# Optimization experiments

Measured on AMD Instinct MI355X. Metric: run time of the kernel, lower is better.

## Reference

```python
import jax, jax.numpy as jnp
import numpy as np

N = 10000   # num_nodes
E = 320000  # num_edges
D = 256     # feature / hidden dim
H = 256


def adj_lap(edge_index, n):
    """Dense normalized adjacency (gcn_norm, no self loops) and sym Laplacian."""
    row, col = edge_index[0], edge_index[1]
    # dense 0/1 adjacency (duplicate edges overwrite with same value, as in the loop)
    A = jnp.zeros((n, n), dtype=jnp.float32).at[row, col].set(1.0)
    # gcn_norm: deg = scatter(w, col) -> column sums
    deg_c = A.sum(axis=0)
    dinv_c = jnp.where(deg_c > 0, jax.lax.rsqrt(jnp.maximum(deg_c, 1e-12)), 0.0)
    anorm = dinv_c[:, None] * A * dinv_c[None, :]
    # get_laplacian 'sym': deg = scatter(w, row) -> row sums; L = I - D^-1/2 A D^-1/2
    deg_r = A.sum(axis=1)
    dinv_r = jnp.where(deg_r > 0, jax.lax.rsqrt(jnp.maximum(deg_r, 1e-12)), 0.0)
    lap = jnp.eye(n, dtype=jnp.float32) - dinv_r[:, None] * A * dinv_r[None, :]
    return lap, anorm


def gcn2(x, M, W1, b1, W2, b2):
    # pretrain_model: two-layer spectral GCN using propagation matrix M
    h = jax.nn.relu(M @ (x @ W1) + b1)
    return M @ (h @ W2) + b2


def setup_inputs() -> dict:
    key = jax.random.key(0)
    k1, k2, k3, k4 = jax.random.split(key, 4)
    x = jax.random.normal(k1, (N, D), dtype=jnp.float32)
    edge_index = jax.random.randint(k2, (2, E), 0, N, dtype=jnp.int64)
    W1 = jax.random.normal(k3, (D, H), dtype=jnp.float32) * 0.05
    b1 = jnp.zeros((H,), dtype=jnp.float32)
    W2 = jax.random.normal(k4, (H, H), dtype=jnp.float32) * 0.05
    b2 = jnp.zeros((H,), dtype=jnp.float32)
    return {"x": x, "edge_index": edge_index, "W1": W1, "b1": b1, "W2": W2, "b2": b2}


def reference(x, edge_index, W1, b1, W2, b2):
    # identity augmentor: x1 = x2 = x, edge_index1 = edge_index2 = edge_index,
    # so adj_lap is identical for both branches (computed once).
    lsym, anorm = adj_lap(edge_index, x.shape[0])
    z1 = gcn2(x, lsym, W1, b1, W2, b2)   # 'high' pass
    z2 = gcn2(x, anorm, W1, b1, W2, b2)  # 'low' pass
    z = z2
    return (z, z1, z2)
```

## Files before the change

### kernel.cpp

```cpp
#include <hip/hip_runtime.h>

#define NN 10000
#define EE 320000
#define HH 256
#define BKT 192

typedef __attribute__((ext_vector_type(8))) short bf16x8;
typedef __attribute__((ext_vector_type(4))) float f32x4;
typedef __attribute__((ext_vector_type(2))) float f32x2;

__device__ float bf2f(unsigned int v) {
    return __uint_as_float(v << 16);
}
__device__ unsigned short f2bf(float f) {
    unsigned int i = __float_as_uint(f);
    return (unsigned short)((i + 0x7fffu + ((i >> 16) & 1u)) >> 16);
}
__device__ unsigned int fp8e(float f) {
    float a = fabsf(f);
    a = fminf(a, 448.0f);
    unsigned int bits = __float_as_uint(a * __uint_as_float(0x03800000u));
    bits = bits + 0x7ffffu + ((bits >> 20) & 1u);
    unsigned int r = bits >> 20;
    if (r > 0x7eu) r = 0x7eu;
    return r | ((__float_as_uint(f) >> 24) & 0x80u);
}
__device__ float fp8d(unsigned int b) {
    float mag = __uint_as_float((b & 0x7fu) << 20) * __uint_as_float(0x7B800000u);
    return __uint_as_float(((b & 0x80u) << 24) | __float_as_uint(mag));
}
__device__ __forceinline__ void fp8dec4(unsigned int g, float* o) {
#if __has_builtin(__builtin_amdgcn_cvt_pk_f32_fp8)
    f32x2 lo = __builtin_amdgcn_cvt_pk_f32_fp8((int)g, false);
    f32x2 hi = __builtin_amdgcn_cvt_pk_f32_fp8((int)g, true);
    o[0] = lo.x; o[1] = lo.y; o[2] = hi.x; o[3] = hi.y;
#else
    #pragma unroll
    for (int j = 0; j < 4; j++) o[j] = fp8d((g >> (8 * j)) & 0xffu);
#endif
}
__device__ unsigned int pk2(unsigned short a, unsigned short b) {
    return (unsigned int)a | ((unsigned int)b << 16);
}
__device__ int eload(const void* ei, int is64, int idx) {
    if (is64) return (int)(((const long long*)ei)[idx]);
    return ((const int*)ei)[idx];
}
__device__ __forceinline__ float dinv_of(int d) {
    return d > 0 ? rsqrtf((float)d) : 0.0f;
}

__global__ void k_A(const void* x, const void* ei, const void* W1, const void* W2,
                    int* flags, int* rawcnt, unsigned short* W1sw,
                    unsigned short* W2sw) {
    int b = blockIdx.x, t = threadIdx.x;
    if (b >= 65) {
        int idx = (b - 65) * 256 + t;
        ((uint4*)rawcnt)[idx] = make_uint4(0, 0, 0, 0);
        return;
    }
    if (b == 0) {
        __shared__ int s0, s1;
        if (t == 0) { s0 = 0; s1 = 0; }
        __syncthreads();
        if (t < 64) {
            const unsigned int* eu = (const unsigned int*)ei;
            const unsigned int* xu = (const unsigned int*)x;
            for (int k = t; k < 256; k += 64)
                if (eu[2 * k + 1] != 0) atomicOr(&s0, 1);
            unsigned int lo = xu[t] & 0xffffu;
            unsigned int ex = (lo >> 7) & 0xffu;
            if (lo == 0u || (ex >= 90u && ex <= 150u)) atomicAdd(&s1, 1);
        }
        __syncthreads();
        if (t == 0) {
            flags[0] = s0 ? 0 : 1;
            flags[1] = (s1 >= 56) ? 0 : 1;
        }
        return;
    }
    __shared__ int plaus;
    if (t == 0) plaus = 0;
    __syncthreads();
    if (t < 64) {
        unsigned int lo = ((const unsigned int*)x)[t] & 0xffffu;
        unsigned int ex = (lo >> 7) & 0xffu;
        if (lo == 0u || (ex >= 90u && ex <= 150u)) atomicAdd(&plaus, 1);
    }
    __syncthreads();
    int f32io = (plaus >= 56) ? 0 : 1;
    int vb = b - 1;
    const void* W = (vb < 32) ? W1 : W2;
    unsigned short* O = (vb < 32) ? W1sw : W2sw;
    int g = ((vb < 32) ? vb : vb - 32) * 256 + t;
    int gl = g & 63;
    int n = (g >> 6) & 15;
    int ks = g >> 10;
    int coln = n * 16 + (gl & 15);
    int krow = ks * 32 + ((gl >> 4) & 3) * 8;
    unsigned short v[8];
    if (f32io) {
        const float* Wf = (const float*)W;
        #pragma unroll
        for (int j = 0; j < 8; j++) v[j] = f2bf(Wf[(size_t)(krow + j) * HH + coln]);
    } else {
        const unsigned short* Wh = (const unsigned short*)W;
        #pragma unroll
        for (int j = 0; j < 8; j++) v[j] = Wh[(size_t)(krow + j) * HH + coln];
    }
    uint4 p;
    p.x = pk2(v[0], v[1]); p.y = pk2(v[2], v[3]);
    p.z = pk2(v[4], v[5]); p.w = pk2(v[6], v[7]);
    *(uint4*)(O + (size_t)g * 8) = p;
}

__global__ void k_B(const void* x, const void* ei, const unsigned short* W1sw,
                    const int* flags, int* rawcnt, unsigned short* bucket,
                    unsigned char* Yf8, void* Oout) {
    int b = blockIdx.x;
    int tid = threadIdx.x;
    if (b >= 625) {
        int e = (b - 625) * 256 + tid;
        if (e >= EE) return;
        int is64 = flags[0];
        int r = eload(ei, is64, e);
        int c = eload(ei, is64, EE + e);
        if (r < 0 || r >= NN || c < 0 || c >= NN) return;
        int slot = atomicAdd(&rawcnt[r], 1);
        if (slot < BKT) bucket[(size_t)r * BKT + slot] = (unsigned short)c;
        return;
    }
    __shared__ unsigned short As[16][264];
    int r0 = b * 16;
    int af32 = flags[1];
    {
        int row = tid >> 4, seg = tid & 15;
        if (af32) {
            const float* ap = (const float*)x + (size_t)(r0 + row) * HH + seg * 16;
            unsigned short v[16];
            #pragma unroll
            for (int j = 0; j < 16; j += 4) {
                float4 q = *(const float4*)(ap + j);
                v[j] = f2bf(q.x); v[j + 1] = f2bf(q.y);
                v[j + 2] = f2bf(q.z); v[j + 3] = f2bf(q.w);
            }
            uint4 p0, p1;
            p0.x = pk2(v[0], v[1]);   p0.y = pk2(v[2], v[3]);
            p0.z = pk2(v[4], v[5]);   p0.w = pk2(v[6], v[7]);
            p1.x = pk2(v[8], v[9]);   p1.y = pk2(v[10], v[11]);
            p1.z = pk2(v[12], v[13]); p1.w = pk2(v[14], v[15]);
            *(uint4*)&As[row][seg * 16] = p0;
            *(uint4*)&As[row][seg * 16 + 8] = p1;
        } else {
            const unsigned short* ap = (const unsigned short*)x + (size_t)(r0 + row) * HH + seg * 16;
            *(uint4*)&As[row][seg * 16] = *(const uint4*)ap;
            *(uint4*)&As[row][seg * 16 + 8] = *(const uint4*)(ap + 8);
        }
    }
    __syncthreads();
    int wv = tid >> 6;
    int lane = tid & 63;
    int quad = lane >> 4;
    int l16 = lane & 15;
    f32x4 acc[4] = {{0,0,0,0},{0,0,0,0},{0,0,0,0},{0,0,0,0}};
    for (int ks = 0; ks < 8; ks++) {
        bf16x8 af = *(const bf16x8*)&As[l16][ks * 32 + quad * 8];
        #pragma unroll
        for (int t = 0; t < 4; t++) {
            int n = wv * 4 + t;
            bf16x8 bf = *(const bf16x8*)(W1sw + ((size_t)(ks * 16 + n) * 64 + lane) * 8);
            acc[t] = __builtin_amdgcn_mfma_f32_16x16x32_bf16(af, bf, acc[t], 0, 0, 0);
        }
    }
    size_t chunkW = (size_t)NN * HH;
    #pragma unroll
    for (int t = 0; t < 4; t++) {
        int cn = (wv * 4 + t) * 16 + l16;
        #pragma unroll
        for (int r = 0; r < 4; r++) {
            int row = r0 + quad * 4 + r;
            float vv = acc[t][r];
            size_t idx = (size_t)row * HH + cn;
            Yf8[idx] = (unsigned char)fp8e(vv);
            if (af32) ((float*)Oout)[2 * chunkW + idx] = vv;
            else      ((unsigned short*)Oout)[2 * chunkW + idx] = f2bf(vv);
        }
    }
}

__global__ void k_DD(const int* rawcnt, int* cnt2, unsigned short* bucket) {
    __shared__ unsigned int bm[4][316];
    __shared__ int cnt[4];
    int wave = threadIdx.x >> 6;
    int lane = threadIdx.x & 63;
    int i = blockIdx.x * 4 + wave;
    int d = rawcnt[i];
    if (d > BKT) d = BKT;
    for (int t = lane; t < 313; t += 64) bm[wave][t] = 0u;
    if (lane == 0) cnt[wave] = 0;
    unsigned short* bp = bucket + (size_t)i * BKT;
    int cvals[3];
    int nt = 0;
    for (int t = lane; t < d; t += 64) cvals[nt++] = (int)bp[t];
    for (int k = 0; k < nt; k++) {
        int c = cvals[k];
        unsigned int m = 1u << (c & 31);
        unsigned int old = atomicOr(&bm[wave][c >> 5], m);
        if (!(old & m)) {
            int p = atomicAdd(&cnt[wave], 1);
            bp[p] = (unsigned short)c;
            atomicAdd(&cnt2[2 * c + 1], 1);
        }
    }
    if (lane == 0) atomicExch(&cnt2[2 * i], cnt[wave]);
}

__global__ __launch_bounds__(512, 8) void k_CD(
        const unsigned char* Yf8, const unsigned short* bucket,
        const int* cnt2, const unsigned short* W2sw, const void* b1,
        const int* flags, unsigned char* G12f8, void* Oout) {
    __shared__ unsigned short Hs[16][264];
    int tid = threadIdx.x;
    int wave = tid >> 6;
    int lane = tid & 63;
    int fb = lane * 4;
    int bbase = blockIdx.x * 8;
    int f32io = flags[1];
    size_t chunkW = (size_t)NN * HH;
    float bv[4];
    if (f32io) {
        const float* bp = (const float*)b1 + fb;
        #pragma unroll
        for (int k = 0; k < 4; k++) bv[k] = bp[k];
    } else {
        uint2 br = *(const uint2*)((const unsigned short*)b1 + fb);
        bv[0] = bf2f(br.x & 0xffffu); bv[1] = bf2f(br.x >> 16);
        bv[2] = bf2f(br.y & 0xffffu); bv[3] = bf2f(br.y >> 16);
    }
    {
        int i = bbase + wave;
        float a1[4] = {0, 0, 0, 0};
        float a2[4] = {0, 0, 0, 0};
        int2 ddi = *(const int2*)(cnt2 + 2 * i);
        int n = ddi.x;
        const unsigned short* cp = bucket + (size_t)i * BKT;
        int t = 0;
        for (; t + 4 <= n; t += 4) {
            ushort4 c4 = *(const ushort4*)(cp + t);
            int cx[4] = {(int)c4.x, (int)c4.y, (int)c4.z, (int)c4.w};
            float wx[4], wy[4];
            #pragma unroll
            for (int j = 0; j < 4; j++) {
                int2 dd = *(const int2*)(cnt2 + 2 * cx[j]);
                wx[j] = dinv_of(dd.x);
                wy[j] = dinv_of(dd.y);
            }
            unsigned int gv[4];
            #pragma unroll
            for (int j = 0; j < 4; j++)
                gv[j] = *(const unsigned int*)(Yf8 + (size_t)cx[j] * 256 + fb);
            #pragma unroll
            for (int j = 0; j < 4; j++) {
                float y[4];
                fp8dec4(gv[j], y);
                #pragma unroll
                for (int k = 0; k < 4; k++) {
                    a1[k] += wx[j] * y[k];
                    a2[k] += wy[j] * y[k];
                }
            }
        }
        for (; t < n; t++) {
            int c = (int)cp[t];
            int2 dd = *(const int2*)(cnt2 + 2 * c);
            float wx = dinv_of(dd.x);
            float wy = dinv_of(dd.y);
            unsigned int g = *(const unsigned int*)(Yf8 + (size_t)c * 256 + fb);
            float y[4];
            fp8dec4(g, y);
            #pragma unroll
            for (int k = 0; k < 4; k++) {
                a1[k] += wx * y[k];
                a2[k] += wy * y[k];
            }
        }
        float wiix = dinv_of(ddi.x);
        float wiiy = dinv_of(ddi.y);
        float yv[4];
        if (f32io) {
            const float* sp = (const float*)Oout + 2 * chunkW + (size_t)i * HH + fb;
            #pragma unroll
            for (int k = 0; k < 4; k++) yv[k] = sp[k];
        } else {
            uint2 yi = *(const uint2*)((const unsigned short*)Oout + 2 * chunkW + (size_t)i * HH + fb);
            yv[0] = bf2f(yi.x & 0xffffu); yv[1] = bf2f(yi.x >> 16);
            yv[2] = bf2f(yi.y & 0xffffu); yv[3] = bf2f(yi.y >> 16);
        }
        float h1[4], h2[4];
        #pragma unroll
        for (int k = 0; k < 4; k++) {
            h1[k] = fmaxf(0.f, yv[k] - wiix * a1[k] + bv[k]);
            h2[k] = fmaxf(0.f, wiiy * a2[k] + bv[k]);
        }
        uint2 p1, p2;
        p1.x = pk2(f2bf(h1[0]), f2bf(h1[1])); p1.y = pk2(f2bf(h1[2]), f2bf(h1[3]));
        p2.x = pk2(f2bf(h2[0]), f2bf(h2[1])); p2.y = pk2(f2bf(h2[2]), f2bf(h2[3]));
        *(uint2*)&Hs[wave][fb] = p1;
        *(uint2*)&Hs[8 + wave][fb] = p2;
    }
    __syncthreads();
    int quad = lane >> 4;
    int l16 = lane & 15;
    f32x4 acc[2] = {{0,0,0,0},{0,0,0,0}};
    for (int ks = 0; ks < 8; ks++) {
        bf16x8 af = *(const bf16x8*)&Hs[l16][ks * 32 + quad * 8];
        #pragma unroll
        for (int t = 0; t < 2; t++) {
            int n = wave * 2 + t;
            bf16x8 bf = *(const bf16x8*)(W2sw + ((size_t)(ks * 16 + n) * 64 + lane) * 8);
            acc[t] = __builtin_amdgcn_mfma_f32_16x16x32_bf16(af, bf, acc[t], 0, 0, 0);
        }
    }
    #pragma unroll
    for (int t = 0; t < 2; t++) {
        int cn = (wave * 2 + t) * 16 + l16;
        #pragma unroll
        for (int r = 0; r < 4; r++) {
            int row16 = quad * 4 + r;
            float vv = acc[t][r];
            if (row16 < 8) {
                int node = bbase + row16;
                G12f8[(size_t)node * 512 + cn] = (unsigned char)fp8e(vv);
                size_t idx = (size_t)node * HH + cn;
                if (f32io) ((float*)Oout)[chunkW + idx] = vv;
                else       ((unsigned short*)Oout)[chunkW + idx] = f2bf(vv);
            } else {
                int node = bbase + row16 - 8;
                G12f8[(size_t)node * 512 + 256 + cn] = (unsigned char)fp8e(vv);
            }
        }
    }
}

__global__ void k_E(const unsigned char* G12f8, const unsigned short* bucket,
                    const int* cnt2, const void* bias, const int* flags,
                    void* Oout) {
    int wave = threadIdx.x >> 6;
    int lane = threadIdx.x & 63;
    int half = lane >> 5;
    int sub = lane & 31;
    int fb = sub * 8;
    int goff = half * 256 + fb;
    int i = blockIdx.x * 4 + wave;
    float acc[8] = {0, 0, 0, 0, 0, 0, 0, 0};
    int2 ddi = *(const int2*)(cnt2 + 2 * i);
    int n = ddi.x;
    const unsigned short* cp = bucket + (size_t)i * BKT;
    int t = 0;
    for (; t + 4 <= n; t += 4) {
        ushort4 c4 = *(const ushort4*)(cp + t);
        int cx[4] = {(int)c4.x, (int)c4.y, (int)c4.z, (int)c4.w};
        float ws[4];
        #pragma unroll
        for (int j = 0; j < 4; j++) {
            int2 dd = *(const int2*)(cnt2 + 2 * cx[j]);
            ws[j] = dinv_of(half ? dd.y : dd.x);
        }
        uint2 gv[4];
        #pragma unroll
        for (int j = 0; j < 4; j++)
            gv[j] = *(const uint2*)(G12f8 + (size_t)cx[j] * 512 + goff);
        #pragma unroll
        for (int j = 0; j < 4; j++) {
            float y[4], y2[4];
            fp8dec4(gv[j].x, y);
            fp8dec4(gv[j].y, y2);
            #pragma unroll
            for (int k = 0; k < 4; k++) {
                acc[k]     += ws[j] * y[k];
                acc[4 + k] += ws[j] * y2[k];
            }
        }
    }
    for (; t < n; t++) {
        int c = (int)cp[t];
        int2 dd = *(const int2*)(cnt2 + 2 * c);
        float wsel = dinv_of(half ? dd.y : dd.x);
        uint2 g = *(const uint2*)(G12f8 + (size_t)c * 512 + goff);
        float y[4], y2[4];
        fp8dec4(g.x, y);
        fp8dec4(g.y, y2);
        #pragma unroll
        for (int k = 0; k < 4; k++) {
            acc[k]     += wsel * y[k];
            acc[4 + k] += wsel * y2[k];
        }
    }
    int f32io = flags[1];
    float bv[8];
    if (f32io) {
        const float* bp = (const float*)bias + fb;
        #pragma unroll
        for (int k = 0; k < 8; k++) bv[k] = bp[k];
    } else {
        uint4 br = *(const uint4*)((const unsigned short*)bias + fb);
        bv[0] = bf2f(br.x & 0xffffu); bv[1] = bf2f(br.x >> 16);
        bv[2] = bf2f(br.y & 0xffffu); bv[3] = bf2f(br.y >> 16);
        bv[4] = bf2f(br.z & 0xffffu); bv[5] = bf2f(br.z >> 16);
        bv[6] = bf2f(br.w & 0xffffu); bv[7] = bf2f(br.w >> 16);
    }
    size_t base = (size_t)i * HH + fb;
    size_t chunkW = (size_t)NN * HH;
    float z[8];
    if (half == 0) {
        float wiix = dinv_of(ddi.x);
        float gvv[8];
        if (f32io) {
            const float* sp = (const float*)Oout + chunkW + base;
            #pragma unroll
            for (int k = 0; k < 8; k++) gvv[k] = sp[k];
        } else {
            uint4 gi = *(const uint4*)((const unsigned short*)Oout + chunkW + base);
            gvv[0] = bf2f(gi.x & 0xffffu); gvv[1] = bf2f(gi.x >> 16);
            gvv[2] = bf2f(gi.y & 0xffffu); gvv[3] = bf2f(gi.y >> 16);
            gvv[4] = bf2f(gi.z & 0xffffu); gvv[5] = bf2f(gi.z >> 16);
            gvv[6] = bf2f(gi.w & 0xffffu); gvv[7] = bf2f(gi.w >> 16);
        }
        #pragma unroll
        for (int k = 0; k < 8; k++) z[k] = gvv[k] - wiix * acc[k] + bv[k];
        if (f32io) {
            float* o = (float*)Oout + chunkW + base;
            *(float4*)o = make_float4(z[0], z[1], z[2], z[3]);
            *(float4*)(o + 4) = make_float4(z[4], z[5], z[6], z[7]);
        } else {
            uint4 p;
            p.x = pk2(f2bf(z[0]), f2bf(z[1])); p.y = pk2(f2bf(z[2]), f2bf(z[3]));
            p.z = pk2(f2bf(z[4]), f2bf(z[5])); p.w = pk2(f2bf(z[6]), f2bf(z[7]));
            *(uint4*)((unsigned short*)Oout + chunkW + base) = p;
        }
    } else {
        float wiiy = dinv_of(ddi.y);
        #pragma unroll
        for (int k = 0; k < 8; k++) z[k] = wiiy * acc[k] + bv[k];
        if (f32io) {
            float* o0 = (float*)Oout + base;
            float* o2 = (float*)Oout + 2 * chunkW + base;
            float4 pa = make_float4(z[0], z[1], z[2], z[3]);
            float4 pb = make_float4(z[4], z[5], z[6], z[7]);
            *(float4*)o0 = pa; *(float4*)(o0 + 4) = pb;
            *(float4*)o2 = pa; *(float4*)(o2 + 4) = pb;
        } else {
            uint4 p;
            p.x = pk2(f2bf(z[0]), f2bf(z[1])); p.y = pk2(f2bf(z[2]), f2bf(z[3]));
            p.z = pk2(f2bf(z[4]), f2bf(z[5])); p.w = pk2(f2bf(z[6]), f2bf(z[7]));
            *(uint4*)((unsigned short*)Oout + base) = p;
            *(uint4*)((unsigned short*)Oout + 2 * chunkW + base) = p;
        }
    }
}

extern "C" void kernel_launch(void* const* d_in, const int* in_sizes, int n_in,
                              void* d_out, int out_size, void* d_ws, size_t ws_size,
                              hipStream_t stream) {
    const void* x = 0; const void* ei = 0;
    const void* W1 = 0; const void* b1 = 0; const void* W2 = 0; const void* b2 = 0;
    for (int i = 0; i < n_in; i++) {
        int s = in_sizes[i];
        if (s == NN * HH) x = d_in[i];
        else if (s == 2 * EE) ei = d_in[i];
        else if (s == HH * HH) { if (!W1) W1 = d_in[i]; else W2 = d_in[i]; }
        else if (s == HH) { if (!b1) b1 = d_in[i]; else b2 = d_in[i]; }
    }

    char* ws = (char*)d_ws;
    size_t off = 0;
    int* flags = (int*)(ws + off); off += 256;
    int* rawcnt = (int*)(ws + off); off += 40960;
    int* cnt2 = (int*)(ws + off); off += 81920;
    unsigned short* bucket = (unsigned short*)(ws + off); off += (size_t)NN * BKT * 2;
    unsigned short* W1sw = (unsigned short*)(ws + off); off += (size_t)HH * HH * 2;
    unsigned short* W2sw = (unsigned short*)(ws + off); off += (size_t)HH * HH * 2;
    unsigned char* Yf8 = (unsigned char*)(ws + off); off += (size_t)NN * 256;
    unsigned char* G12f8 = (unsigned char*)(ws + off); off += (size_t)NN * 512;

    k_A<<<95, 256, 0, stream>>>(x, ei, W1, W2, flags, rawcnt, W1sw, W2sw);
    k_B<<<1875, 256, 0, stream>>>(x, ei, W1sw, flags, rawcnt, bucket, Yf8, d_out);
    k_DD<<<NN / 4, 256, 0, stream>>>(rawcnt, cnt2, bucket);
    k_CD<<<NN / 8, 512, 0, stream>>>(Yf8, bucket, cnt2, W2sw, b1, flags, G12f8, d_out);
    k_E<<<NN / 4, 256, 0, stream>>>(G12f8, bucket, cnt2, b2, flags, d_out);
}
```

Baseline: 184.0 us.

## Restructure kernel pipeline: merge bucketing into prep, dedup with GEMM, pack fp8 stores

The edge bucketing now runs in the first kernel, which detects the index width itself, and rawcnt/cnt2 are zeroed by a memset. The dedup pass is folded into the X@W1 GEMM kernel, so the pipeline drops from five launches to four plus the memset. It also adds packed two-value fp8 conversion for the epilogue stores, unrolls the gather loops by 8 with loads issued earlier, and lowers the launch-bounds occupancy hint for k_CD and k_E. Each bucketing block now rereads the edge-index probe, and merging heterogeneous work into one kernel can unbalance scheduling.

```diff
diff --git a/kernel.cpp b/kernel.cpp
--- a/kernel.cpp
+++ b/kernel.cpp
@@ -39,6 +39,13 @@
     for (int j = 0; j < 4; j++) o[j] = fp8d((g >> (8 * j)) & 0xffu);
 #endif
 }
+__device__ __forceinline__ unsigned int fp8e2(float a, float b) {
+#if __has_builtin(__builtin_amdgcn_cvt_pk_fp8_f32)
+    return (unsigned int)__builtin_amdgcn_cvt_pk_fp8_f32(a, b, 0, false);
+#else
+    return fp8e(a) | (fp8e(b) << 8);
+#endif
+}
 __device__ unsigned int pk2(unsigned short a, unsigned short b) {
     return (unsigned int)a | ((unsigned int)b << 16);
 }
@@ -50,13 +57,28 @@
     return d > 0 ? rsqrtf((float)d) : 0.0f;
 }
 
-__global__ void k_A(const void* x, const void* ei, const void* W1, const void* W2,
-                    int* flags, int* rawcnt, unsigned short* W1sw,
-                    unsigned short* W2sw) {
+__global__ void k_AB(const void* x, const void* ei, const void* W1, const void* W2,
+                     int* flags, int* rawcnt, unsigned short* bucket,
+                     unsigned short* W1sw, unsigned short* W2sw) {
     int b = blockIdx.x, t = threadIdx.x;
     if (b >= 65) {
-        int idx = (b - 65) * 256 + t;
-        ((uint4*)rawcnt)[idx] = make_uint4(0, 0, 0, 0);
+        __shared__ int s_nz;
+        if (t == 0) s_nz = 0;
+        __syncthreads();
+        if (t < 64) {
+            const unsigned int* eu = (const unsigned int*)ei;
+            for (int k = t; k < 256; k += 64)
+                if (eu[2 * k + 1] != 0) atomicOr(&s_nz, 1);
+        }
+        __syncthreads();
+        int is64 = s_nz ? 0 : 1;
+        int e = (b - 65) * 256 + t;
+        if (e >= EE) return;
+        int r = eload(ei, is64, e);
+        int c = eload(ei, is64, EE + e);
+        if (r < 0 || r >= NN || c < 0 || c >= NN) return;
+        int slot = atomicAdd(&rawcnt[r], 1);
+        if (slot < BKT) bucket[(size_t)r * BKT + slot] = (unsigned short)c;
         return;
     }
     if (b == 0) {
@@ -114,24 +136,40 @@
     *(uint4*)(O + (size_t)g * 8) = p;
 }
 
-__global__ void k_B(const void* x, const void* ei, const unsigned short* W1sw,
-                    const int* flags, int* rawcnt, unsigned short* bucket,
-                    unsigned char* Yf8, void* Oout) {
+__global__ void k_DG(const void* x, const unsigned short* W1sw, const int* flags,
+                     const int* rawcnt, int* cnt2, unsigned short* bucket,
+                     unsigned char* Yf8, void* Oout) {
+    __shared__ unsigned int bm[4][316];
+    __shared__ int cnt[4];
+    __shared__ unsigned short As[16][264];
     int b = blockIdx.x;
     int tid = threadIdx.x;
-    if (b >= 625) {
-        int e = (b - 625) * 256 + tid;
-        if (e >= EE) return;
-        int is64 = flags[0];
-        int r = eload(ei, is64, e);
-        int c = eload(ei, is64, EE + e);
-        if (r < 0 || r >= NN || c < 0 || c >= NN) return;
-        int slot = atomicAdd(&rawcnt[r], 1);
-        if (slot < BKT) bucket[(size_t)r * BKT + slot] = (unsigned short)c;
+    if (b < 2500) {
+        int wave = tid >> 6;
+        int lane = tid & 63;
+        int i = b * 4 + wave;
+        int d = rawcnt[i];
+        if (d > BKT) d = BKT;
+        for (int t = lane; t < 313; t += 64) bm[wave][t] = 0u;
+        if (lane == 0) cnt[wave] = 0;
+        unsigned short* bp = bucket + (size_t)i * BKT;
+        int cvals[3];
+        int nt = 0;
+        for (int t = lane; t < d; t += 64) cvals[nt++] = (int)bp[t];
+        for (int k = 0; k < nt; k++) {
+            int c = cvals[k];
+            unsigned int m = 1u << (c & 31);
+            unsigned int old = atomicOr(&bm[wave][c >> 5], m);
+            if (!(old & m)) {
+                int p = atomicAdd(&cnt[wave], 1);
+                bp[p] = (unsigned short)c;
+                atomicAdd(&cnt2[2 * c + 1], 1);
+            }
+        }
+        if (lane == 0) atomicExch(&cnt2[2 * i], cnt[wave]);
         return;
     }
-    __shared__ unsigned short As[16][264];
-    int r0 = b * 16;
+    int r0 = (b - 2500) * 16;
     int af32 = flags[1];
     {
         int row = tid >> 4, seg = tid & 15;
@@ -177,45 +215,26 @@
     for (int t = 0; t < 4; t++) {
         int cn = (wv * 4 + t) * 16 + l16;
         #pragma unroll
-        for (int r = 0; r < 4; r++) {
+        for (int r = 0; r < 4; r += 2) {
             int row = r0 + quad * 4 + r;
-            float vv = acc[t][r];
-            size_t idx = (size_t)row * HH + cn;
-            Yf8[idx] = (unsigned char)fp8e(vv);
-            if (af32) ((float*)Oout)[2 * chunkW + idx] = vv;
-            else      ((unsigned short*)Oout)[2 * chunkW + idx] = f2bf(vv);
-        }
-    }
-}
-
-__global__ void k_DD(const int* rawcnt, int* cnt2, unsigned short* bucket) {
-    __shared__ unsigned int bm[4][316];
-    __shared__ int cnt[4];
-    int wave = threadIdx.x >> 6;
-    int lane = threadIdx.x & 63;
-    int i = blockIdx.x * 4 + wave;
-    int d = rawcnt[i];
-    if (d > BKT) d = BKT;
-    for (int t = lane; t < 313; t += 64) bm[wave][t] = 0u;
-    if (lane == 0) cnt[wave] = 0;
-    unsigned short* bp = bucket + (size_t)i * BKT;
-    int cvals[3];
-    int nt = 0;
-    for (int t = lane; t < d; t += 64) cvals[nt++] = (int)bp[t];
-    for (int k = 0; k < nt; k++) {
-        int c = cvals[k];
-        unsigned int m = 1u << (c & 31);
-        unsigned int old = atomicOr(&bm[wave][c >> 5], m);
-        if (!(old & m)) {
-            int p = atomicAdd(&cnt[wave], 1);
-            bp[p] = (unsigned short)c;
-            atomicAdd(&cnt2[2 * c + 1], 1);
-        }
-    }
-    if (lane == 0) atomicExch(&cnt2[2 * i], cnt[wave]);
-}
-
-__global__ __launch_bounds__(512, 8) void k_CD(
+            float v0 = acc[t][r], v1 = acc[t][r + 1];
+            unsigned int pk = fp8e2(v0, v1);
+            size_t idx0 = (size_t)row * HH + cn;
+            size_t idx1 = idx0 + HH;
+            Yf8[idx0] = (unsigned char)(pk & 0xffu);
+            Yf8[idx1] = (unsigned char)((pk >> 8) & 0xffu);
+            if (af32) {
+                ((float*)Oout)[2 * chunkW + idx0] = v0;
+                ((float*)Oout)[2 * chunkW + idx1] = v1;
+            } else {
+                ((unsigned short*)Oout)[2 * chunkW + idx0] = f2bf(v0);
+                ((unsigned short*)Oout)[2 * chunkW + idx1] = f2bf(v1);
+            }
+        }
+    }
+}
+
+__global__ __launch_bounds__(512, 4) void k_CD(
         const unsigned char* Yf8, const unsigned short* bucket,
         const int* cnt2, const unsigned short* W2sw, const void* b1,
         const int* flags, unsigned char* G12f8, void* Oout) {
@@ -245,9 +264,40 @@
         int n = ddi.x;
         const unsigned short* cp = bucket + (size_t)i * BKT;
         int t = 0;
+        for (; t + 8 <= n; t += 8) {
+            ushort4 ca = *(const ushort4*)(cp + t);
+            ushort4 cb = *(const ushort4*)(cp + t + 4);
+            int cx[8] = {(int)ca.x, (int)ca.y, (int)ca.z, (int)ca.w,
+                         (int)cb.x, (int)cb.y, (int)cb.z, (int)cb.w};
+            unsigned int gv[8];
+            #pragma unroll
+            for (int j = 0; j < 8; j++)
+                gv[j] = *(const unsigned int*)(Yf8 + (size_t)cx[j] * 256 + fb);
+            float wx[8], wy[8];
+            #pragma unroll
+            for (int j = 0; j < 8; j++) {
+                int2 dd = *(const int2*)(cnt2 + 2 * cx[j]);
+                wx[j] = dinv_of(dd.x);
+                wy[j] = dinv_of(dd.y);
+            }
+            #pragma unroll
+            for (int j = 0; j < 8; j++) {
+                float y[4];
+                fp8dec4(gv[j], y);
+                #pragma unroll
+                for (int k = 0; k < 4; k++) {
+                    a1[k] += wx[j] * y[k];
+                    a2[k] += wy[j] * y[k];
+                }
+            }
+        }
         for (; t + 4 <= n; t += 4) {
             ushort4 c4 = *(const ushort4*)(cp + t);
             int cx[4] = {(int)c4.x, (int)c4.y, (int)c4.z, (int)c4.w};
+            unsigned int gv[4];
+            #pragma unroll
+            for (int j = 0; j < 4; j++)
+                gv[j] = *(const unsigned int*)(Yf8 + (size_t)cx[j] * 256 + fb);
             float wx[4], wy[4];
             #pragma unroll
             for (int j = 0; j < 4; j++) {
@@ -255,10 +305,6 @@
                 wx[j] = dinv_of(dd.x);
                 wy[j] = dinv_of(dd.y);
             }
-            unsigned int gv[4];
-            #pragma unroll
-            for (int j = 0; j < 4; j++)
-                gv[j] = *(const unsigned int*)(Yf8 + (size_t)cx[j] * 256 + fb);
             #pragma unroll
             for (int j = 0; j < 4; j++) {
                 float y[4];
@@ -325,26 +371,35 @@
     for (int t = 0; t < 2; t++) {
         int cn = (wave * 2 + t) * 16 + l16;
         #pragma unroll
-        for (int r = 0; r < 4; r++) {
+        for (int r = 0; r < 4; r += 2) {
             int row16 = quad * 4 + r;
-            float vv = acc[t][r];
+            float v0 = acc[t][r], v1 = acc[t][r + 1];
+            unsigned int pk = fp8e2(v0, v1);
             if (row16 < 8) {
                 int node = bbase + row16;
-                G12f8[(size_t)node * 512 + cn] = (unsigned char)fp8e(vv);
-                size_t idx = (size_t)node * HH + cn;
-                if (f32io) ((float*)Oout)[chunkW + idx] = vv;
-                else       ((unsigned short*)Oout)[chunkW + idx] = f2bf(vv);
+                G12f8[(size_t)node * 512 + cn] = (unsigned char)(pk & 0xffu);
+                G12f8[(size_t)(node + 1) * 512 + cn] = (unsigned char)((pk >> 8) & 0xffu);
+                size_t idx0 = (size_t)node * HH + cn;
+                size_t idx1 = idx0 + HH;
+                if (f32io) {
+                    ((float*)Oout)[chunkW + idx0] = v0;
+                    ((float*)Oout)[chunkW + idx1] = v1;
+                } else {
+                    ((unsigned short*)Oout)[chunkW + idx0] = f2bf(v0);
+                    ((unsigned short*)Oout)[chunkW + idx1] = f2bf(v1);
+                }
             } else {
                 int node = bbase + row16 - 8;
-                G12f8[(size_t)node * 512 + 256 + cn] = (unsigned char)fp8e(vv);
-            }
-        }
-    }
-}
-
-__global__ void k_E(const unsigned char* G12f8, const unsigned short* bucket,
-                    const int* cnt2, const void* bias, const int* flags,
-                    void* Oout) {
+                G12f8[(size_t)node * 512 + 256 + cn] = (unsigned char)(pk & 0xffu);
+                G12f8[(size_t)(node + 1) * 512 + 256 + cn] = (unsigned char)((pk >> 8) & 0xffu);
+            }
+        }
+    }
+}
+
+__global__ __launch_bounds__(256, 4) void k_E(
+        const unsigned char* G12f8, const unsigned short* bucket,
+        const int* cnt2, const void* bias, const int* flags, void* Oout) {
     int wave = threadIdx.x >> 6;
     int lane = threadIdx.x & 63;
     int half = lane >> 5;
@@ -357,19 +412,46 @@
     int n = ddi.x;
     const unsigned short* cp = bucket + (size_t)i * BKT;
     int t = 0;
+    for (; t + 8 <= n; t += 8) {
+        ushort4 ca = *(const ushort4*)(cp + t);
+        ushort4 cb = *(const ushort4*)(cp + t + 4);
+        int cx[8] = {(int)ca.x, (int)ca.y, (int)ca.z, (int)ca.w,
+                     (int)cb.x, (int)cb.y, (int)cb.z, (int)cb.w};
+        uint2 gv[8];
+        #pragma unroll
+        for (int j = 0; j < 8; j++)
+            gv[j] = *(const uint2*)(G12f8 + (size_t)cx[j] * 512 + goff);
+        float ws[8];
+        #pragma unroll
+        for (int j = 0; j < 8; j++) {
+            int2 dd = *(const int2*)(cnt2 + 2 * cx[j]);
+            ws[j] = dinv_of(half ? dd.y : dd.x);
+        }
+        #pragma unroll
+        for (int j = 0; j < 8; j++) {
+            float y[4], y2[4];
+            fp8dec4(gv[j].x, y);
+            fp8dec4(gv[j].y, y2);
+            #pragma unroll
+            for (int k = 0; k < 4; k++) {
+                acc[k]     += ws[j] * y[k];
+                acc[4 + k] += ws[j] * y2[k];
+            }
+        }
+    }
     for (; t + 4 <= n; t += 4) {
         ushort4 c4 = *(const ushort4*)(cp + t);
         int cx[4] = {(int)c4.x, (int)c4.y, (int)c4.z, (int)c4.w};
+        uint2 gv[4];
+        #pragma unroll
+        for (int j = 0; j < 4; j++)
+            gv[j] = *(const uint2*)(G12f8 + (size_t)cx[j] * 512 + goff);
         float ws[4];
         #pragma unroll
         for (int j = 0; j < 4; j++) {
             int2 dd = *(const int2*)(cnt2 + 2 * cx[j]);
             ws[j] = dinv_of(half ? dd.y : dd.x);
         }
-        uint2 gv[4];
-        #pragma unroll
-        for (int j = 0; j < 4; j++)
-            gv[j] = *(const uint2*)(G12f8 + (size_t)cx[j] * 512 + goff);
         #pragma unroll
         for (int j = 0; j < 4; j++) {
             float y[4], y2[4];
@@ -483,9 +565,11 @@
     unsigned char* Yf8 = (unsigned char*)(ws + off); off += (size_t)NN * 256;
     unsigned char* G12f8 = (unsigned char*)(ws + off); off += (size_t)NN * 512;
 
-    k_A<<<95, 256, 0, stream>>>(x, ei, W1, W2, flags, rawcnt, W1sw, W2sw);
-    k_B<<<1875, 256, 0, stream>>>(x, ei, W1sw, flags, rawcnt, bucket, Yf8, d_out);
-    k_DD<<<NN / 4, 256, 0, stream>>>(rawcnt, cnt2, bucket);
+    hipMemsetAsync(rawcnt, 0, 40960 + 81920, stream);
+    k_AB<<<65 + EE / 256, 256, 0, stream>>>(x, ei, W1, W2, flags, rawcnt, bucket,
+                                            W1sw, W2sw);
+    k_DG<<<2500 + 625, 256, 0, stream>>>(x, W1sw, flags, rawcnt, cnt2, bucket,
+                                         Yf8, d_out);
     k_CD<<<NN / 8, 512, 0, stream>>>(Yf8, bucket, cnt2, W2sw, b1, flags, G12f8, d_out);
     k_E<<<NN / 4, 256, 0, stream>>>(G12f8, bucket, cnt2, b2, flags, d_out);
 }
```

Measured after the change: 186.2 us. Within noise of the previous version (+1.2%).
